# Optimization experiments

Measured on AMD Instinct MI355X. Metric: run time of the kernel, lower is better.

## Reference

```python
import jax, jax.numpy as jnp
import numpy as np

D_MODEL = 256
NHEAD = 8
HEAD_DIM = D_MODEL // NHEAD
CLIP = 10.0
LN_EPS = 1e-5


def setup_inputs() -> dict:
    key = jax.random.key(0)
    ks = jax.random.split(key, 10)
    B, N, d = 2, 256, D_MODEL
    s = 1.0 / np.sqrt(d)
    return {
        "nodes": jax.random.normal(ks[0], (B, N, d), jnp.float32),
        "edges": jax.random.normal(ks[1], (B, N, N, d), jnp.float32),
        # shared projection (used for Q, K, V, edge-Q, edge-K, output)
        "W": jax.random.normal(ks[2], (d, d), jnp.float32) * s,
        "b": jax.random.normal(ks[3], (d,), jnp.float32) * 0.01,
        # shared LayerNorm params (same module applied twice)
        "ln_g": jnp.ones((d,), jnp.float32),
        "ln_b": jnp.zeros((d,), jnp.float32),
        # feedforward
        "W1": jax.random.normal(ks[4], (d, 4 * d), jnp.float32) * s,
        "b1": jnp.zeros((4 * d,), jnp.float32),
        "W2": jax.random.normal(ks[5], (4 * d, d), jnp.float32) * (1.0 / np.sqrt(4 * d)),
        "b2": jnp.zeros((d,), jnp.float32),
    }


def _layer_norm(x, g, b):
    mu = jnp.mean(x, axis=-1, keepdims=True)
    var = jnp.var(x, axis=-1, keepdims=True)
    return (x - mu) * jax.lax.rsqrt(var + LN_EPS) * g + b


def reference(nodes, edges, W, b, ln_g, ln_b, W1, b1, W2, b2):
    B, N, d = nodes.shape
    h, hd = NHEAD, HEAD_DIM

    x = _layer_norm(nodes, ln_g, ln_b)

    # Node projections (shared weight -> q == k == v)
    nq = (x @ W + b).reshape(B, N, h, hd)
    nk = nq
    nv = nq

    # Edge projections (shared weight -> eq == ek)
    eq = (edges @ W + b).reshape(B, N, N, h, hd)
    ek = eq

    # Broadcast-add node+edge queries/keys: [B, N, N, h, hd]
    query = eq + nq[:, :, None, :, :]
    key = ek + nk[:, None, :, :, :]

    scores = jnp.einsum("bijhd,bijhd->bhij", query, key) / np.sqrt(hd)
    scores = CLIP * jnp.tanh(scores)
    attn = jax.nn.softmax(scores, axis=-1)  # [B, h, N, N]

    # attn @ V: [B, h, N, hd] -> [B, N, d]
    out = jnp.einsum("bhij,bjhd->bihd", attn, nv).reshape(B, N, d)
    out = out @ W + b

    x = x + out
    x = _layer_norm(x, ln_g, ln_b)
    ff = jax.nn.gelu(x @ W1 + b1, approximate=False) @ W2 + b2
    return ff + x
```

## Files before the change

### kernel.cpp

```cpp
#include <hip/hip_runtime.h>

typedef _Float16 half_t;
typedef __attribute__((ext_vector_type(8))) _Float16 f16x8;
typedef __attribute__((ext_vector_type(4))) float f32x4;

#define DM 256
#define NH 8
#define NN 256
#define NB 2
#define JT 32

__global__ __launch_bounds__(1024) void k_ln_proj(
    const float* __restrict__ nodes, const float* __restrict__ W,
    const float* __restrict__ bias, const float* __restrict__ ln_g,
    const float* __restrict__ ln_b, float* __restrict__ xs,
    float* __restrict__ nqv, float* __restrict__ nqvpb) {
  __shared__ float sx[2][DM];
  __shared__ float pp[4][2][DM];
  __shared__ float rs[8], rq[8];
  const int t = threadIdx.x;
  const int r0 = blockIdx.x * 2;
  const int row = t >> 8, col = t & 255;
  float v = 0.f;
  if (t < 512) v = nodes[(size_t)(r0 + row) * DM + col];
  float s = v, q = v * v;
#pragma unroll
  for (int m = 1; m <= 32; m <<= 1) {
    s += __shfl_xor(s, m, 64);
    q += __shfl_xor(q, m, 64);
  }
  if (t < 512 && (t & 63) == 0) { rs[t >> 6] = s; rq[t >> 6] = q; }
  __syncthreads();
  if (t < 512) {
    int rb = row * 4;
    float ss = rs[rb] + rs[rb + 1] + rs[rb + 2] + rs[rb + 3];
    float qq = rq[rb] + rq[rb + 1] + rq[rb + 2] + rq[rb + 3];
    float mu = ss * (1.f / DM);
    float var = qq * (1.f / DM) - mu * mu;
    float xv = (v - mu) * rsqrtf(var + 1e-5f) * ln_g[col] + ln_b[col];
    sx[row][col] = xv;
    xs[(size_t)(r0 + row) * DM + col] = xv;
  }
  __syncthreads();
  const int rg = t >> 8;
  float a0 = 0.f, a1 = 0.f;
#pragma unroll 8
  for (int kk = 0; kk < 64; ++kk) {
    int k = rg * 64 + kk;
    float wv = W[(size_t)k * DM + col];
    a0 += sx[0][k] * wv;
    a1 += sx[1][k] * wv;
  }
  pp[rg][0][col] = a0;
  pp[rg][1][col] = a1;
  __syncthreads();
  if (t < 512) {
    float bb = bias[col];
    float r = pp[0][row][col] + pp[1][row][col] + pp[2][row][col] +
              pp[3][row][col] + bb;
    nqv[(size_t)(r0 + row) * DM + col] = r;
    nqvpb[(size_t)(r0 + row) * DM + col] = r + bb;
  }
}

__global__ __launch_bounds__(256) void k_wt16(const float* __restrict__ W,
                                              half_t* __restrict__ WT) {
  int c = blockIdx.x, t = threadIdx.x;
  WT[c * DM + t] = (half_t)W[t * DM + c];
}

__global__ __launch_bounds__(256, 4) void k_edge_scores(
    const float* __restrict__ edges, const half_t* __restrict__ WT,
    const float* __restrict__ nqvpb, float* __restrict__ scores) {
  __shared__ __align__(16) char smem[4096 + 32 * 1040];
  const int tid = threadIdx.x;
  const int l = tid & 63;
  const int w = tid >> 6;
  const int idx = blockIdx.x;
  const int jb = idx & 7;
  const int i = (idx >> 3) & (NN - 1);
  const int b = idx >> 11;
  const int j0 = jb * JT;

  float* nlds = (float*)(smem + 4096);

  const float* nb_ = nqvpb + ((size_t)(b * NN) + j0) * DM;
#pragma unroll
  for (int p = 0; p < 8; ++p) {
    int u = p * 256 + tid;
    int row = u >> 6, c4 = u & 63;
    f32x4 v = *(const f32x4*)(nb_ + (size_t)row * DM + c4 * 4);
    *(f32x4*)(nlds + row * 260 + c4 * 4) = v;
  }

  f32x4 acc[4][2];
#pragma unroll
  for (int ct = 0; ct < 4; ++ct)
#pragma unroll
    for (int jt = 0; jt < 2; ++jt) acc[ct][jt] = (f32x4){0.f, 0.f, 0.f, 0.f};

  const float* eg = edges + ((size_t)(b * NN + i) * NN + j0) * DM;
  const int f4 = tid & 15, row0 = tid >> 4;
  const char* wtb = (const char*)WT;

  f32x4 pe[2];
  pe[0] = *(const f32x4*)(eg + row0 * DM + f4 * 4);
  pe[1] = *(const f32x4*)(eg + (row0 + 16) * DM + f4 * 4);

  for (int kc = 0; kc < 4; ++kc) {
    f16x8 wf[2][4];
#pragma unroll
    for (int ks = 0; ks < 2; ++ks)
#pragma unroll
      for (int ct = 0; ct < 4; ++ct) {
        int c = w * 64 + ct * 16 + (l & 15);
        wf[ks][ct] = *(const f16x8*)(wtb + c * 512 + kc * 128 + ks * 64 +
                                     ((l >> 4) * 16));
      }
#pragma unroll
    for (int q = 0; q < 2; ++q) {
      int row = row0 + q * 16;
      union { unsigned long long u; half_t h[4]; } a1;
#pragma unroll
      for (int z = 0; z < 4; ++z) a1.h[z] = (half_t)pe[q][z];
      int off = (row * 128 + f4 * 8) ^ ((row & 7) << 4);
      *(unsigned long long*)(smem + off) = a1.u;
    }
    __syncthreads();
    if (kc < 3) {
      pe[0] = *(const f32x4*)(eg + row0 * DM + (kc + 1) * 64 + f4 * 4);
      pe[1] = *(const f32x4*)(eg + (row0 + 16) * DM + (kc + 1) * 64 + f4 * 4);
    }
#pragma unroll
    for (int ks = 0; ks < 2; ++ks) {
      f16x8 fq[2];
#pragma unroll
      for (int jt = 0; jt < 2; ++jt) {
        int r = jt * 16 + (l & 15);
        int off = (r * 128 + ks * 64 + ((l >> 4) * 16)) ^ ((r & 7) << 4);
        fq[jt] = *(const f16x8*)(smem + off);
      }
#pragma unroll
      for (int ct = 0; ct < 4; ++ct)
#pragma unroll
        for (int jt = 0; jt < 2; ++jt)
          acc[ct][jt] = __builtin_amdgcn_mfma_f32_16x16x32_f16(
              wf[ks][ct], fq[jt], acc[ct][jt], 0, 0, 0);
    }
    __syncthreads();
  }

  const float* qrow = nqvpb + ((size_t)(b * NN) + i) * DM;
  const float scale = 0.17677669529663687f;
#pragma unroll
  for (int a = 0; a < 2; ++a) {
    float s0 = 0.f, s1 = 0.f;
#pragma unroll
    for (int u = 0; u < 2; ++u) {
      int ct = a * 2 + u;
      int cbase = w * 64 + ct * 16 + ((l >> 4) * 4);
      f32x4 qi = *(const f32x4*)(qrow + cbase);
      f32x4 k0 = *(const f32x4*)(nlds + (l & 15) * 260 + cbase);
      f32x4 k1 = *(const f32x4*)(nlds + (16 + (l & 15)) * 260 + cbase);
#pragma unroll
      for (int rr = 0; rr < 4; ++rr) {
        s0 += (acc[ct][0][rr] + qi[rr]) * (acc[ct][0][rr] + k0[rr]);
        s1 += (acc[ct][1][rr] + qi[rr]) * (acc[ct][1][rr] + k1[rr]);
      }
    }
#pragma unroll
    for (int jt = 0; jt < 2; ++jt) {
      float sv = jt ? s1 : s0;
      sv += __shfl_xor(sv, 16, 64);
      sv += __shfl_xor(sv, 32, 64);
      float sc = 10.0f * tanhf(sv * scale);
      if (l < 16) {
        int h = w * 2 + a;
        int jg = j0 + jt * 16 + l;
        scores[(((size_t)(b * NH) + h) * NN + i) * NN + jg] = sc;
      }
    }
  }
}

__global__ __launch_bounds__(1024) void k_attn_out(
    const float* __restrict__ scores, const float* __restrict__ nqv,
    const float* __restrict__ W, const float* __restrict__ bias,
    const float* __restrict__ xs, const float* __restrict__ ln_g,
    const float* __restrict__ ln_b, float* __restrict__ ys) {
  __shared__ float sp[NH * NN];
  __shared__ float pp[4][256];
  __shared__ float aor[256];
  __shared__ float rs[4], rq[4];
  const int t = threadIdx.x;
  const int b = blockIdx.x >> 8, i = blockIdx.x & 255;
#pragma unroll
  for (int p = 0; p < 2; ++p) {
    int idx2 = p * 1024 + t;
    sp[idx2] = scores[(((size_t)(b * NH) + (idx2 >> 8)) * NN + i) * NN + (idx2 & 255)];
  }
  __syncthreads();
  const int w = t >> 6, l = t & 63;
  if (w < 8) {
    f32x4 v = *(f32x4*)(sp + w * NN + l * 4);
    float m = fmaxf(fmaxf(v[0], v[1]), fmaxf(v[2], v[3]));
#pragma unroll
    for (int mm = 1; mm <= 32; mm <<= 1) m = fmaxf(m, __shfl_xor(m, mm, 64));
    v[0] = __expf(v[0] - m); v[1] = __expf(v[1] - m);
    v[2] = __expf(v[2] - m); v[3] = __expf(v[3] - m);
    float s = v[0] + v[1] + v[2] + v[3];
#pragma unroll
    for (int mm = 1; mm <= 32; mm <<= 1) s += __shfl_xor(s, mm, 64);
    float inv = 1.0f / s;
    v[0] *= inv; v[1] *= inv; v[2] *= inv; v[3] *= inv;
    *(f32x4*)(sp + w * NN + l * 4) = v;
  }
  __syncthreads();
  const int d = t & 255, kg = t >> 8, h = d >> 5;
  const float* vb = nqv + (size_t)b * NN * DM;
  float acc = 0.f;
#pragma unroll 8
  for (int jj = 0; jj < 64; ++jj) {
    int j = kg * 64 + jj;
    acc += sp[h * 256 + j] * vb[(size_t)j * DM + d];
  }
  pp[kg][d] = acc;
  __syncthreads();
  if (t < 256) aor[t] = pp[0][t] + pp[1][t] + pp[2][t] + pp[3][t];
  __syncthreads();
  float a0 = 0.f;
#pragma unroll 8
  for (int kk = 0; kk < 64; ++kk) {
    int k = kg * 64 + kk;
    a0 += aor[k] * W[(size_t)k * DM + d];
  }
  pp[kg][d] = a0;
  __syncthreads();
  float val = 0.f;
  if (t < 256)
    val = pp[0][t] + pp[1][t] + pp[2][t] + pp[3][t] + bias[t] +
          xs[((size_t)(b * NN) + i) * DM + t];
  float s2 = val, q2 = val * val;
#pragma unroll
  for (int m = 1; m <= 32; m <<= 1) {
    s2 += __shfl_xor(s2, m, 64);
    q2 += __shfl_xor(q2, m, 64);
  }
  if (t < 256 && l == 0) { rs[w] = s2; rq[w] = q2; }
  __syncthreads();
  if (t < 256) {
    float ss = rs[0] + rs[1] + rs[2] + rs[3];
    float qq = rq[0] + rq[1] + rq[2] + rq[3];
    float mu = ss * (1.f / DM);
    float var = qq * (1.f / DM) - mu * mu;
    ys[((size_t)(b * NN) + i) * DM + t] =
        (val - mu) * rsqrtf(var + 1e-5f) * ln_g[t] + ln_b[t];
  }
}

__global__ __launch_bounds__(1024) void k_ffn(const float* __restrict__ ys,
                                              const float* __restrict__ W1,
                                              const float* __restrict__ b1,
                                              const float* __restrict__ W2,
                                              const float* __restrict__ b2,
                                              float* __restrict__ out) {
  __shared__ float sy[2][DM];
  __shared__ float sg[2][1024];
  __shared__ float pp[4][2][256];
  const int t = threadIdx.x;
  const int r0 = blockIdx.x * 2;
  if (t < 512) sy[t >> 8][t & 255] = ys[(size_t)(r0 + (t >> 8)) * DM + (t & 255)];
  __syncthreads();
  float a0 = b1[t], a1 = a0;
#pragma unroll 8
  for (int k = 0; k < DM; ++k) {
    float wv = W1[(size_t)k * 1024 + t];
    a0 += sy[0][k] * wv;
    a1 += sy[1][k] * wv;
  }
  sg[0][t] = 0.5f * a0 * (1.0f + erff(a0 * 0.70710678118654752f));
  sg[1][t] = 0.5f * a1 * (1.0f + erff(a1 * 0.70710678118654752f));
  __syncthreads();
  const int kg = t >> 8, col = t & 255;
  float z0 = 0.f, z1 = 0.f;
#pragma unroll 8
  for (int kk = 0; kk < 256; ++kk) {
    int k = kg * 256 + kk;
    float wv = W2[(size_t)k * 256 + col];
    z0 += sg[0][k] * wv;
    z1 += sg[1][k] * wv;
  }
  pp[kg][0][col] = z0;
  pp[kg][1][col] = z1;
  __syncthreads();
  if (t < 512) {
    int row = t >> 8;
    float r = pp[0][row][col] + pp[1][row][col] + pp[2][row][col] +
              pp[3][row][col] + b2[col] + sy[row][col];
    out[(size_t)(r0 + row) * DM + col] = r;
  }
}

extern "C" void kernel_launch(void* const* d_in, const int* in_sizes, int n_in,
                              void* d_out, int out_size, void* d_ws, size_t ws_size,
                              hipStream_t stream) {
  const float* nodes = (const float*)d_in[0];
  const float* edges = (const float*)d_in[1];
  const float* W     = (const float*)d_in[2];
  const float* bias  = (const float*)d_in[3];
  const float* ln_g  = (const float*)d_in[4];
  const float* ln_b  = (const float*)d_in[5];
  const float* W1    = (const float*)d_in[6];
  const float* b1    = (const float*)d_in[7];
  const float* W2    = (const float*)d_in[8];
  const float* b2    = (const float*)d_in[9];
  float* out = (float*)d_out;

  char* ws = (char*)d_ws;
  float*  xs     = (float*)(ws + 0x000000);
  float*  nqv    = (float*)(ws + 0x080000);
  float*  nqvpb  = (float*)(ws + 0x100000);
  half_t* WT16   = (half_t*)(ws + 0x180000);
  float*  scores = (float*)(ws + 0x1A0000);
  float*  ys     = (float*)(ws + 0x5A0000);

  k_ln_proj<<<NB * NN / 2, 1024, 0, stream>>>(nodes, W, bias, ln_g, ln_b, xs, nqv, nqvpb);
  k_wt16<<<DM, 256, 0, stream>>>(W, WT16);
  k_edge_scores<<<NB * NN * (NN / JT), 256, 0, stream>>>(edges, WT16, nqvpb, scores);
  k_attn_out<<<NB * NN, 1024, 0, stream>>>(scores, nqv, W, bias, xs, ln_g, ln_b, ys);
  k_ffn<<<NB * NN / 2, 1024, 0, stream>>>(ys, W1, b1, W2, b2, out);
}
```

Before: 309.3 us.

## Use transposed fp16 weights in node GEMVs and prefetch all edge tiles upfront

A single prep kernel now converts W, W1 and W2 into transposed fp16 copies. The node projection, attention output projection and FFN GEMVs read these with 16-byte vector loads and vectorized shared-memory reads, halving weight bytes and cutting per-element load instructions. The edge-score kernel issues all four k-chunk global loads of its edge tile before the main loop instead of double-buffering one chunk ahead, which exposes more memory parallelism at the cost of extra registers. Converting weights to fp16 also lowers precision in the node-side GEMVs.

```diff
diff --git a/kernel.cpp b/kernel.cpp
--- a/kernel.cpp
+++ b/kernel.cpp
@@ -10,8 +10,30 @@
 #define NB 2
 #define JT 32
 
+__global__ __launch_bounds__(256) void k_prep(const float* __restrict__ W,
+                                              const float* __restrict__ W1,
+                                              const float* __restrict__ W2,
+                                              half_t* __restrict__ WT,
+                                              half_t* __restrict__ W1T,
+                                              half_t* __restrict__ W2T) {
+  const int t = threadIdx.x, bid = blockIdx.x;
+  if (bid < 256) {
+    WT[bid * 256 + t] = (half_t)W[(size_t)t * 256 + bid];
+  } else if (bid < 1280) {
+    int m = bid - 256;
+    W1T[(size_t)m * 256 + t] = (half_t)W1[(size_t)t * 1024 + m];
+  } else {
+    int n = bid - 1280;
+#pragma unroll
+    for (int j = 0; j < 4; ++j) {
+      int k = j * 256 + t;
+      W2T[(size_t)n * 1024 + k] = (half_t)W2[(size_t)k * 256 + n];
+    }
+  }
+}
+
 __global__ __launch_bounds__(1024) void k_ln_proj(
-    const float* __restrict__ nodes, const float* __restrict__ W,
+    const float* __restrict__ nodes, const half_t* __restrict__ WT,
     const float* __restrict__ bias, const float* __restrict__ ln_g,
     const float* __restrict__ ln_b, float* __restrict__ xs,
     float* __restrict__ nqv, float* __restrict__ nqvpb) {
@@ -44,12 +66,21 @@
   __syncthreads();
   const int rg = t >> 8;
   float a0 = 0.f, a1 = 0.f;
-#pragma unroll 8
-  for (int kk = 0; kk < 64; ++kk) {
-    int k = rg * 64 + kk;
-    float wv = W[(size_t)k * DM + col];
-    a0 += sx[0][k] * wv;
-    a1 += sx[1][k] * wv;
+#pragma unroll
+  for (int k8 = 0; k8 < 8; ++k8) {
+    int k = rg * 64 + k8 * 8;
+    f16x8 wv = *(const f16x8*)(WT + (size_t)col * 256 + k);
+    f32x4 xa0 = *(const f32x4*)(&sx[0][k]);
+    f32x4 xb0 = *(const f32x4*)(&sx[0][k + 4]);
+    f32x4 xa1 = *(const f32x4*)(&sx[1][k]);
+    f32x4 xb1 = *(const f32x4*)(&sx[1][k + 4]);
+#pragma unroll
+    for (int z = 0; z < 4; ++z) {
+      a0 += xa0[z] * (float)wv[z];
+      a0 += xb0[z] * (float)wv[z + 4];
+      a1 += xa1[z] * (float)wv[z];
+      a1 += xb1[z] * (float)wv[z + 4];
+    }
   }
   pp[rg][0][col] = a0;
   pp[rg][1][col] = a1;
@@ -61,12 +92,6 @@
     nqv[(size_t)(r0 + row) * DM + col] = r;
     nqvpb[(size_t)(r0 + row) * DM + col] = r + bb;
   }
-}
-
-__global__ __launch_bounds__(256) void k_wt16(const float* __restrict__ W,
-                                              half_t* __restrict__ WT) {
-  int c = blockIdx.x, t = threadIdx.x;
-  WT[c * DM + t] = (half_t)W[t * DM + c];
 }
 
 __global__ __launch_bounds__(256, 4) void k_edge_scores(
@@ -82,8 +107,17 @@
   const int b = idx >> 11;
   const int j0 = jb * JT;
 
+  const float* eg = edges + ((size_t)(b * NN + i) * NN + j0) * DM;
+  const int f4 = tid & 15, row0 = tid >> 4;
+
+  f32x4 pe[4][2];
+#pragma unroll
+  for (int kc = 0; kc < 4; ++kc) {
+    pe[kc][0] = *(const f32x4*)(eg + row0 * DM + kc * 64 + f4 * 4);
+    pe[kc][1] = *(const f32x4*)(eg + (row0 + 16) * DM + kc * 64 + f4 * 4);
+  }
+
   float* nlds = (float*)(smem + 4096);
-
   const float* nb_ = nqvpb + ((size_t)(b * NN) + j0) * DM;
 #pragma unroll
   for (int p = 0; p < 8; ++p) {
@@ -99,14 +133,9 @@
 #pragma unroll
     for (int jt = 0; jt < 2; ++jt) acc[ct][jt] = (f32x4){0.f, 0.f, 0.f, 0.f};
 
-  const float* eg = edges + ((size_t)(b * NN + i) * NN + j0) * DM;
-  const int f4 = tid & 15, row0 = tid >> 4;
   const char* wtb = (const char*)WT;
 
-  f32x4 pe[2];
-  pe[0] = *(const f32x4*)(eg + row0 * DM + f4 * 4);
-  pe[1] = *(const f32x4*)(eg + (row0 + 16) * DM + f4 * 4);
-
+#pragma unroll
   for (int kc = 0; kc < 4; ++kc) {
     f16x8 wf[2][4];
 #pragma unroll
@@ -122,15 +151,11 @@
       int row = row0 + q * 16;
       union { unsigned long long u; half_t h[4]; } a1;
 #pragma unroll
-      for (int z = 0; z < 4; ++z) a1.h[z] = (half_t)pe[q][z];
+      for (int z = 0; z < 4; ++z) a1.h[z] = (half_t)pe[kc][q][z];
       int off = (row * 128 + f4 * 8) ^ ((row & 7) << 4);
       *(unsigned long long*)(smem + off) = a1.u;
     }
     __syncthreads();
-    if (kc < 3) {
-      pe[0] = *(const f32x4*)(eg + row0 * DM + (kc + 1) * 64 + f4 * 4);
-      pe[1] = *(const f32x4*)(eg + (row0 + 16) * DM + (kc + 1) * 64 + f4 * 4);
-    }
 #pragma unroll
     for (int ks = 0; ks < 2; ++ks) {
       f16x8 fq[2];
@@ -185,7 +210,7 @@
 
 __global__ __launch_bounds__(1024) void k_attn_out(
     const float* __restrict__ scores, const float* __restrict__ nqv,
-    const float* __restrict__ W, const float* __restrict__ bias,
+    const half_t* __restrict__ WT, const float* __restrict__ bias,
     const float* __restrict__ xs, const float* __restrict__ ln_g,
     const float* __restrict__ ln_b, float* __restrict__ ys) {
   __shared__ float sp[NH * NN];
@@ -229,10 +254,15 @@
   if (t < 256) aor[t] = pp[0][t] + pp[1][t] + pp[2][t] + pp[3][t];
   __syncthreads();
   float a0 = 0.f;
-#pragma unroll 8
-  for (int kk = 0; kk < 64; ++kk) {
-    int k = kg * 64 + kk;
-    a0 += aor[k] * W[(size_t)k * DM + d];
+#pragma unroll
+  for (int k8 = 0; k8 < 8; ++k8) {
+    int k = kg * 64 + k8 * 8;
+    f16x8 wv = *(const f16x8*)(WT + (size_t)d * 256 + k);
+    f32x4 ya = *(const f32x4*)(&aor[k]);
+    f32x4 yb = *(const f32x4*)(&aor[k + 4]);
+#pragma unroll
+    for (int z = 0; z < 4; ++z)
+      a0 += ya[z] * (float)wv[z] + yb[z] * (float)wv[z + 4];
   }
   pp[kg][d] = a0;
   __syncthreads();
@@ -259,9 +289,9 @@
 }
 
 __global__ __launch_bounds__(1024) void k_ffn(const float* __restrict__ ys,
-                                              const float* __restrict__ W1,
+                                              const half_t* __restrict__ W1T,
                                               const float* __restrict__ b1,
-                                              const float* __restrict__ W2,
+                                              const half_t* __restrict__ W2T,
                                               const float* __restrict__ b2,
                                               float* __restrict__ out) {
   __shared__ float sy[2][DM];
@@ -272,23 +302,42 @@
   if (t < 512) sy[t >> 8][t & 255] = ys[(size_t)(r0 + (t >> 8)) * DM + (t & 255)];
   __syncthreads();
   float a0 = b1[t], a1 = a0;
-#pragma unroll 8
-  for (int k = 0; k < DM; ++k) {
-    float wv = W1[(size_t)k * 1024 + t];
-    a0 += sy[0][k] * wv;
-    a1 += sy[1][k] * wv;
+#pragma unroll
+  for (int k8 = 0; k8 < 32; ++k8) {
+    int k = k8 * 8;
+    f16x8 wv = *(const f16x8*)(W1T + (size_t)t * 256 + k);
+    f32x4 xa0 = *(const f32x4*)(&sy[0][k]);
+    f32x4 xb0 = *(const f32x4*)(&sy[0][k + 4]);
+    f32x4 xa1 = *(const f32x4*)(&sy[1][k]);
+    f32x4 xb1 = *(const f32x4*)(&sy[1][k + 4]);
+#pragma unroll
+    for (int z = 0; z < 4; ++z) {
+      a0 += xa0[z] * (float)wv[z];
+      a0 += xb0[z] * (float)wv[z + 4];
+      a1 += xa1[z] * (float)wv[z];
+      a1 += xb1[z] * (float)wv[z + 4];
+    }
   }
   sg[0][t] = 0.5f * a0 * (1.0f + erff(a0 * 0.70710678118654752f));
   sg[1][t] = 0.5f * a1 * (1.0f + erff(a1 * 0.70710678118654752f));
   __syncthreads();
   const int kg = t >> 8, col = t & 255;
   float z0 = 0.f, z1 = 0.f;
-#pragma unroll 8
-  for (int kk = 0; kk < 256; ++kk) {
-    int k = kg * 256 + kk;
-    float wv = W2[(size_t)k * 256 + col];
-    z0 += sg[0][k] * wv;
-    z1 += sg[1][k] * wv;
+#pragma unroll
+  for (int k8 = 0; k8 < 32; ++k8) {
+    int k = kg * 256 + k8 * 8;
+    f16x8 wv = *(const f16x8*)(W2T + (size_t)col * 1024 + k);
+    f32x4 ga0 = *(const f32x4*)(&sg[0][k]);
+    f32x4 gb0 = *(const f32x4*)(&sg[0][k + 4]);
+    f32x4 ga1 = *(const f32x4*)(&sg[1][k]);
+    f32x4 gb1 = *(const f32x4*)(&sg[1][k + 4]);
+#pragma unroll
+    for (int z = 0; z < 4; ++z) {
+      z0 += ga0[z] * (float)wv[z];
+      z0 += gb0[z] * (float)wv[z + 4];
+      z1 += ga1[z] * (float)wv[z];
+      z1 += gb1[z] * (float)wv[z + 4];
+    }
   }
   pp[kg][0][col] = z0;
   pp[kg][1][col] = z1;
@@ -323,10 +372,12 @@
   half_t* WT16   = (half_t*)(ws + 0x180000);
   float*  scores = (float*)(ws + 0x1A0000);
   float*  ys     = (float*)(ws + 0x5A0000);
-
-  k_ln_proj<<<NB * NN / 2, 1024, 0, stream>>>(nodes, W, bias, ln_g, ln_b, xs, nqv, nqvpb);
-  k_wt16<<<DM, 256, 0, stream>>>(W, WT16);
+  half_t* W1T16  = (half_t*)(ws + 0x620000);
+  half_t* W2T16  = (half_t*)(ws + 0x6A0000);
+
+  k_prep<<<1536, 256, 0, stream>>>(W, W1, W2, WT16, W1T16, W2T16);
+  k_ln_proj<<<NB * NN / 2, 1024, 0, stream>>>(nodes, WT16, bias, ln_g, ln_b, xs, nqv, nqvpb);
   k_edge_scores<<<NB * NN * (NN / JT), 256, 0, stream>>>(edges, WT16, nqvpb, scores);
-  k_attn_out<<<NB * NN, 1024, 0, stream>>>(scores, nqv, W, bias, xs, ln_g, ln_b, ys);
-  k_ffn<<<NB * NN / 2, 1024, 0, stream>>>(ys, W1, b1, W2, b2, out);
-}
+  k_attn_out<<<NB * NN, 1024, 0, stream>>>(scores, nqv, WT16, bias, xs, ln_g, ln_b, ys);
+  k_ffn<<<NB * NN / 2, 1024, 0, stream>>>(ys, W1T16, b1, W2T16, b2, out);
+}
```

New measurement: 523.1 us. 1.69x slower.
